# Optimization experiments

Measured on AMD Instinct MI355X. Metric: run time of the kernel, lower is better.

The kernel has to match this reference:

```python
import jax, jax.numpy as jnp
import numpy as np

N_NODES = 50000
N_EDGES = 500000
HIDDEN = 64
NUM_BASIS = 32
NUM_SH = 4  # (lmax+1)^2 with lmax=1


def _mlp(x, w1, b1, w2, b2):
    # Linear -> SiLU -> Linear, matching nn.Sequential(Linear, SiLU, Linear)
    return jax.nn.silu(x @ w1 + b1) @ w2 + b2


def setup_inputs() -> dict:
    key = jax.random.key(0)
    ks = jax.random.split(key, 10)
    scale_in = 1.0 / np.sqrt(NUM_BASIS)
    scale_h = 1.0 / np.sqrt(HIDDEN)
    return {
        "scalar": jax.random.normal(ks[0], (N_NODES, HIDDEN), dtype=jnp.float32),
        "vector": jax.random.normal(ks[1], (N_NODES, 3, HIDDEN), dtype=jnp.float32),
        "edge_sh": jax.random.normal(ks[2], (N_EDGES, NUM_SH), dtype=jnp.float32),
        "edge_length": jax.random.uniform(ks[3], (N_EDGES, NUM_BASIS), dtype=jnp.float32),
        "edge_index": jax.random.randint(ks[4], (2, N_EDGES), 0, N_NODES, dtype=jnp.int32),
        "sw1": jax.random.normal(ks[5], (NUM_BASIS, HIDDEN), dtype=jnp.float32) * scale_in,
        "sb1": jnp.zeros((HIDDEN,), dtype=jnp.float32),
        "sw2": jax.random.normal(ks[6], (HIDDEN, HIDDEN), dtype=jnp.float32) * scale_h,
        "sb2": jnp.zeros((HIDDEN,), dtype=jnp.float32),
        "vw1": jax.random.normal(ks[7], (NUM_BASIS, HIDDEN), dtype=jnp.float32) * scale_in,
        "vb1": jnp.zeros((HIDDEN,), dtype=jnp.float32),
        "vw2": jax.random.normal(ks[8], (HIDDEN, HIDDEN), dtype=jnp.float32) * scale_h,
        "vb2": jnp.zeros((HIDDEN,), dtype=jnp.float32),
    }


def reference(scalar, vector, edge_sh, edge_length, edge_index,
              sw1, sb1, sw2, sb2, vw1, vb1, vw2, vb2):
    # edge_sh is accepted (as in the torch forward signature) but unused.
    row, col = edge_index[0], edge_index[1]
    n = scalar.shape[0]

    # Edge-wise MLP weights from radial basis expansion: [E, hidden]
    scalar_weights = _mlp(edge_length, sw1, sb1, sw2, sb2)
    # Gather source-node scalars, weight, scatter-add to destination nodes.
    scalar_msg = scalar[col] * scalar_weights                   # [E, hidden]
    out_scalar = jax.ops.segment_sum(scalar_msg, row, num_segments=n)

    vector_weights = _mlp(edge_length, vw1, vb1, vw2, vb2)      # [E, hidden]
    vector_msg = vector[col] * vector_weights[:, None, :]       # [E, 3, hidden]
    out_vector = jax.ops.segment_sum(vector_msg, row, num_segments=n)

    return out_scalar, out_vector
```

## Files before the change

kernel.cpp:

```cpp
#include <hip/hip_runtime.h>

#define HIDDEN 64
#define NB 32
#define SCAN_BLOCK 1024
#define HSTR 72

typedef __attribute__((ext_vector_type(8))) short bf16x8;
typedef __attribute__((ext_vector_type(4))) float f32x4;

static __device__ __forceinline__ unsigned short f2bf(float x) {
    union { float f; unsigned u; } v; v.f = x;
    unsigned r = v.u + 0x7fffu + ((v.u >> 16) & 1u);
    return (unsigned short)(r >> 16);
}
static __device__ __forceinline__ float bf2f(unsigned short s) {
    union { unsigned u; float f; } v; v.u = ((unsigned)s) << 16;
    return v.f;
}

__global__ __launch_bounds__(256) void featpack_kernel(
    const float* __restrict__ scalar,
    const float* __restrict__ vector,
    ushort4* __restrict__ feat,
    int total)
{
    int i = blockIdx.x * 256 + threadIdx.x;
    if (i >= total) return;
    const int n = i >> 6, l = i & 63;
    const float* vp = vector + (size_t)n * 192 + l;
    ushort4 o;
    o.x = f2bf(scalar[i]);
    o.y = f2bf(vp[0]);
    o.z = f2bf(vp[64]);
    o.w = f2bf(vp[128]);
    feat[i] = o;
}

__global__ __launch_bounds__(SCAN_BLOCK) void scan_pass1(
    const int* __restrict__ counts, int* __restrict__ partial,
    int* __restrict__ blocksums, int N)
{
    __shared__ int tmp[SCAN_BLOCK];
    const int t = threadIdx.x;
    const int gid = blockIdx.x * SCAN_BLOCK + t;
    int v = (gid < N) ? counts[gid] : 0;
    tmp[t] = v;
    __syncthreads();
    for (int off = 1; off < SCAN_BLOCK; off <<= 1) {
        int x = (t >= off) ? tmp[t - off] : 0;
        __syncthreads();
        tmp[t] += x;
        __syncthreads();
    }
    if (gid < N) partial[gid] = tmp[t] - v;
    if (t == SCAN_BLOCK - 1) blocksums[blockIdx.x] = tmp[t];
}

__global__ __launch_bounds__(64) void scan_pass2(int* __restrict__ blocksums, int nb)
{
    const int t = threadIdx.x;
    int v = (t < nb) ? blocksums[t] : 0;
    int s = v;
    #pragma unroll
    for (int off = 1; off < 64; off <<= 1) {
        int x = __shfl_up(s, off, 64);
        if (t >= off) s += x;
    }
    if (t < nb) blocksums[t] = s - v;
}

__global__ __launch_bounds__(SCAN_BLOCK) void scan_pass3(
    const int* __restrict__ partial, const int* __restrict__ blocksums,
    int* __restrict__ offsets, int* __restrict__ cursors, int N, int E)
{
    const int gid = blockIdx.x * SCAN_BLOCK + threadIdx.x;
    if (gid < N) {
        int o = partial[gid] + blocksums[blockIdx.x];
        offsets[gid] = o;
        cursors[gid] = o;
    }
    if (blockIdx.x == 0 && threadIdx.x == 0) offsets[N] = E;
}

__global__ __launch_bounds__(256) void scatter_kernel(
    const int* __restrict__ edge_index, int* __restrict__ cursors,
    int2* __restrict__ pc, int E)
{
    int i = blockIdx.x * 256 + threadIdx.x;
    if (i < E) {
        int pos = atomicAdd(&cursors[edge_index[i]], 1);
        pc[pos] = make_int2(i, edge_index[E + i]);
    }
}

__global__ __launch_bounds__(256) void mlp_mfma_kernel(
    const float* __restrict__ edge_length,
    const int*   __restrict__ edge_index,
    int* __restrict__ counts,
    const float* __restrict__ sw1, const float* __restrict__ sb1,
    const float* __restrict__ sw2, const float* __restrict__ sb2,
    const float* __restrict__ vw1, const float* __restrict__ vb1,
    const float* __restrict__ vw2, const float* __restrict__ vb2,
    unsigned short* __restrict__ W,
    int E, int nchunks)
{
    __shared__ short Hs[4][64 * HSTR];

    const int t    = threadIdx.x;
    const int lane = t & 63;
    const int wid  = t >> 6;
    const int quad = lane >> 4;
    const int l16  = lane & 15;
    short* Hw = Hs[wid];

    const float* w1p[2] = {sw1, vw1};
    const float* b1p[2] = {sb1, vb1};
    const float* w2p[2] = {sw2, vw2};
    const float* b2p[2] = {sb2, vb2};

    bf16x8 w1f[2][4];
    bf16x8 w2f[2][2][4];
    float  b1v[2][4], b2v[2][4];
    #pragma unroll
    for (int m = 0; m < 2; ++m) {
        #pragma unroll
        for (int nt = 0; nt < 4; ++nt) {
            const int col = nt * 16 + l16;
            #pragma unroll
            for (int j = 0; j < 8; ++j)
                w1f[m][nt][j] = (short)f2bf(w1p[m][(quad * 8 + j) * HIDDEN + col]);
            #pragma unroll
            for (int kk = 0; kk < 2; ++kk) {
                #pragma unroll
                for (int j = 0; j < 8; ++j)
                    w2f[m][kk][nt][j] = (short)f2bf(w2p[m][(kk * 32 + quad * 8 + j) * HIDDEN + col]);
            }
            b1v[m][nt] = b1p[m][col];
            b2v[m][nt] = b2p[m][col];
        }
    }

    const int wave_g = blockIdx.x * 4 + wid;
    const int nwaves = gridDim.x * 4;

    for (int c = wave_g; c < nchunks; c += nwaves) {
        const int j0 = c * 64;

        {
            const int e = j0 + lane;
            if (e < E) atomicAdd(&counts[edge_index[e]], 1);
        }

        bf16x8 af[4];
        #pragma unroll
        for (int mt = 0; mt < 4; ++mt) {
            int e = j0 + mt * 16 + l16;
            if (e >= E) e = E - 1;
            const float* r = edge_length + (size_t)e * NB + quad * 8;
            float4 u0 = *(const float4*)r;
            float4 u1 = *(const float4*)(r + 4);
            af[mt][0] = (short)f2bf(u0.x); af[mt][1] = (short)f2bf(u0.y);
            af[mt][2] = (short)f2bf(u0.z); af[mt][3] = (short)f2bf(u0.w);
            af[mt][4] = (short)f2bf(u1.x); af[mt][5] = (short)f2bf(u1.y);
            af[mt][6] = (short)f2bf(u1.z); af[mt][7] = (short)f2bf(u1.w);
        }

        #pragma unroll
        for (int m = 0; m < 2; ++m) {
            #pragma unroll
            for (int mt = 0; mt < 4; ++mt) {
                #pragma unroll
                for (int nt = 0; nt < 4; ++nt) {
                    f32x4 cf = {b1v[m][nt], b1v[m][nt], b1v[m][nt], b1v[m][nt]};
                    cf = __builtin_amdgcn_mfma_f32_16x16x32_bf16(af[mt], w1f[m][nt], cf, 0, 0, 0);
                    #pragma unroll
                    for (int r4 = 0; r4 < 4; ++r4) {
                        float x = cf[r4];
                        x = x / (1.0f + __expf(-x));
                        const int row = mt * 16 + quad * 4 + r4;
                        Hw[row * HSTR + nt * 16 + l16] = (short)f2bf(x);
                    }
                }
            }

            #pragma unroll
            for (int mt = 0; mt < 4; ++mt) {
                const int arow = mt * 16 + l16;
                bf16x8 a0 = *(const bf16x8*)(Hw + arow * HSTR + quad * 8);
                bf16x8 a1 = *(const bf16x8*)(Hw + arow * HSTR + 32 + quad * 8);
                #pragma unroll
                for (int nt = 0; nt < 4; ++nt) {
                    f32x4 cf = {b2v[m][nt], b2v[m][nt], b2v[m][nt], b2v[m][nt]};
                    cf = __builtin_amdgcn_mfma_f32_16x16x32_bf16(a1, w2f[m][1][nt], cf, 0, 0, 0);
                    cf = __builtin_amdgcn_mfma_f32_16x16x32_bf16(a0, w2f[m][0][nt], cf, 0, 0, 0);
                    #pragma unroll
                    for (int r4 = 0; r4 < 4; ++r4) {
                        const int row = mt * 16 + quad * 4 + r4;
                        Hw[row * HSTR + nt * 16 + l16] = (short)f2bf(cf[r4]);
                    }
                }
            }

            #pragma unroll
            for (int i = 0; i < 8; ++i) {
                const int row = i * 8 + (lane >> 3);
                bf16x8 v = *(const bf16x8*)(Hw + row * HSTR + (lane & 7) * 8);
                if (j0 + row < E)
                    *(bf16x8*)(W + (size_t)(j0 + row) * 128 + m * 64 + (lane & 7) * 8) = v;
            }
        }
    }
}

__global__ __launch_bounds__(256) void node_kernel_feat(
    const ushort4* __restrict__ feat,
    const int* __restrict__ offsets,
    const int2* __restrict__ pc,
    const unsigned short* __restrict__ W,
    float* __restrict__ out_scalar,
    float* __restrict__ out_vector,
    int N)
{
    const int lane = threadIdx.x & 63;
    const int wave = blockIdx.x * 4 + (threadIdx.x >> 6);
    const int nw   = gridDim.x * 4;

    for (int n = wave; n < N; n += nw) {
        const int beg = offsets[n];
        const int end = offsets[n + 1];

        float as = 0.0f, a0 = 0.0f, a1 = 0.0f, a2 = 0.0f;
        float ws = 0, wv = 0, s = 0, v0 = 0, v1 = 0, v2 = 0;

        if (beg < end) {
            const int2 p = pc[beg];
            const unsigned short* wp = W + (size_t)p.x * 128;
            ws = bf2f(wp[lane]); wv = bf2f(wp[64 + lane]);
            const ushort4 f = feat[(size_t)p.y * 64 + lane];
            s = bf2f(f.x); v0 = bf2f(f.y); v1 = bf2f(f.z); v2 = bf2f(f.w);
        }

        for (int j = beg; j < end; ++j) {
            const int jn = (j + 1 < end) ? j + 1 : j;
            const int2 p = pc[jn];
            const unsigned short* wp = W + (size_t)p.x * 128;
            const float wsn = bf2f(wp[lane]);
            const float wvn = bf2f(wp[64 + lane]);
            const ushort4 f = feat[(size_t)p.y * 64 + lane];
            const float sn  = bf2f(f.x);
            const float v0n = bf2f(f.y);
            const float v1n = bf2f(f.z);
            const float v2n = bf2f(f.w);

            as = fmaf(s,  ws, as);
            a0 = fmaf(v0, wv, a0);
            a1 = fmaf(v1, wv, a1);
            a2 = fmaf(v2, wv, a2);

            ws = wsn; wv = wvn; s = sn; v0 = v0n; v1 = v1n; v2 = v2n;
        }

        out_scalar[(size_t)n * HIDDEN + lane] = as;
        float* ov = out_vector + (size_t)n * 3 * HIDDEN;
        ov[lane]       = a0;
        ov[64 + lane]  = a1;
        ov[128 + lane] = a2;
    }
}

__global__ __launch_bounds__(256) void node_kernel_f32(
    const float* __restrict__ scalar,
    const float* __restrict__ vector,
    const int* __restrict__ offsets,
    const int2* __restrict__ pc,
    const unsigned short* __restrict__ W,
    float* __restrict__ out_scalar,
    float* __restrict__ out_vector,
    int N)
{
    const int lane = threadIdx.x & 63;
    const int wave = blockIdx.x * 4 + (threadIdx.x >> 6);
    const int nw   = gridDim.x * 4;

    for (int n = wave; n < N; n += nw) {
        const int beg = offsets[n];
        const int end = offsets[n + 1];
        float as = 0.0f, a0 = 0.0f, a1 = 0.0f, a2 = 0.0f;
        for (int j = beg; j < end; ++j) {
            const int2 p = pc[j];
            const unsigned short* wp = W + (size_t)p.x * 128;
            const float w_s = bf2f(wp[lane]);
            const float w_v = bf2f(wp[64 + lane]);
            const float* sp = scalar + (size_t)p.y * HIDDEN;
            const float* vp = vector + (size_t)p.y * 3 * HIDDEN;
            as = fmaf(sp[lane],       w_s, as);
            a0 = fmaf(vp[lane],       w_v, a0);
            a1 = fmaf(vp[64 + lane],  w_v, a1);
            a2 = fmaf(vp[128 + lane], w_v, a2);
        }
        out_scalar[(size_t)n * HIDDEN + lane] = as;
        float* ov = out_vector + (size_t)n * 3 * HIDDEN;
        ov[lane]       = a0;
        ov[64 + lane]  = a1;
        ov[128 + lane] = a2;
    }
}

extern "C" void kernel_launch(void* const* d_in, const int* in_sizes, int n_in,
                              void* d_out, int out_size, void* d_ws, size_t ws_size,
                              hipStream_t stream) {
    const float* scalar      = (const float*)d_in[0];
    const float* vector      = (const float*)d_in[1];
    const float* edge_length = (const float*)d_in[3];
    const int*   edge_index  = (const int*)d_in[4];
    const float* sw1 = (const float*)d_in[5];
    const float* sb1 = (const float*)d_in[6];
    const float* sw2 = (const float*)d_in[7];
    const float* sb2 = (const float*)d_in[8];
    const float* vw1 = (const float*)d_in[9];
    const float* vb1 = (const float*)d_in[10];
    const float* vw2 = (const float*)d_in[11];
    const float* vb2 = (const float*)d_in[12];

    const int N = in_sizes[0] / HIDDEN;
    const int E = in_sizes[4] / 2;

    float* out_scalar = (float*)d_out;
    float* out_vector = (float*)d_out + (size_t)N * HIDDEN;

    size_t off = 0;
    unsigned short* W = (unsigned short*)d_ws;
    off += (size_t)E * 128 * 2;
    int2* pc = (int2*)((char*)d_ws + off);
    off += (size_t)E * 8;
    int* ib = (int*)((char*)d_ws + off);
    int* counts    = ib;
    int* partial   = ib + N;
    int* offsets   = ib + 2 * N;
    int* cursors   = ib + 3 * N + 1;
    int* blocksums = ib + 4 * N + 1;
    off += ((size_t)4 * N + 1 + 64) * 4;
    off = (off + 15) & ~(size_t)15;
    ushort4* feat = (ushort4*)((char*)d_ws + off);
    const bool use_feat = (off + (size_t)N * 64 * 8) <= ws_size;

    hipMemsetAsync(counts, 0, (size_t)N * sizeof(int), stream);

    const int egrid = (E + 255) / 256;

    if (use_feat) {
        const int total = N * 64;
        featpack_kernel<<<(total + 255) / 256, 256, 0, stream>>>(
            scalar, vector, feat, total);
    }

    const int nchunks = (E + 63) / 64;
    mlp_mfma_kernel<<<512, 256, 0, stream>>>(
        edge_length, edge_index, counts,
        sw1, sb1, sw2, sb2, vw1, vb1, vw2, vb2,
        W, E, nchunks);

    const int nb = (N + SCAN_BLOCK - 1) / SCAN_BLOCK;
    scan_pass1<<<nb, SCAN_BLOCK, 0, stream>>>(counts, partial, blocksums, N);
    scan_pass2<<<1, 64, 0, stream>>>(blocksums, nb);
    scan_pass3<<<nb, SCAN_BLOCK, 0, stream>>>(partial, blocksums, offsets, cursors, N, E);
    scatter_kernel<<<egrid, 256, 0, stream>>>(edge_index, cursors, pc, E);

    const int ngrid = (N + 3) / 4;
    if (use_feat) {
        node_kernel_feat<<<ngrid, 256, 0, stream>>>(
            feat, offsets, pc, W, out_scalar, out_vector, N);
    } else {
        node_kernel_f32<<<ngrid, 256, 0, stream>>>(
            scalar, vector, offsets, pc, W, out_scalar, out_vector, N);
    }
}
```

Before: 335.4 us.

## Restructure edge MLP kernel: split MLPs across waves, keep hidden layer in registers

Each block's four waves now split as two chunk slots times two MLPs (scalar or vector), so each wave holds the weights of only one MLP. The GEMMs are transposed (weights as the A operand, edges as B), which lets the first-layer SiLU output be packed straight into bf16 registers as the second GEMM's operand instead of going through LDS. SiLU now uses a hardware reciprocal, bf16 conversion uses packed intrinsics, and the grid covers all chunks (one pass per slot) instead of a fixed 512 blocks. The edge_length loads are duplicated across the two MLP waves, and the approximate reciprocal slightly changes numerics.

```diff
diff --git a/kernel.cpp b/kernel.cpp
--- a/kernel.cpp
+++ b/kernel.cpp
@@ -1,4 +1,5 @@
 #include <hip/hip_runtime.h>
+#include <hip/hip_bf16.h>
 
 #define HIDDEN 64
 #define NB 32
@@ -17,12 +18,18 @@
     union { unsigned u; float f; } v; v.u = ((unsigned)s) << 16;
     return v.f;
 }
+static __device__ __forceinline__ unsigned pk2(float a, float b) {
+    __hip_bfloat162 h = __float22bfloat162_rn(make_float2(a, b));
+    unsigned u; __builtin_memcpy(&u, &h, 4); return u;
+}
+static __device__ __forceinline__ float fast_silu(float x) {
+    float e = __expf(-x);
+    return x * __builtin_amdgcn_rcpf(1.0f + e);
+}
 
 __global__ __launch_bounds__(256) void featpack_kernel(
-    const float* __restrict__ scalar,
-    const float* __restrict__ vector,
-    ushort4* __restrict__ feat,
-    int total)
+    const float* __restrict__ scalar, const float* __restrict__ vector,
+    ushort4* __restrict__ feat, int total)
 {
     int i = blockIdx.x * 256 + threadIdx.x;
     if (i >= total) return;
@@ -109,105 +116,97 @@
     const int t    = threadIdx.x;
     const int lane = t & 63;
     const int wid  = t >> 6;
+    const int slot = wid & 1;
+    const int m    = wid >> 1;
     const int quad = lane >> 4;
     const int l16  = lane & 15;
     short* Hw = Hs[wid];
 
-    const float* w1p[2] = {sw1, vw1};
-    const float* b1p[2] = {sb1, vb1};
-    const float* w2p[2] = {sw2, vw2};
-    const float* b2p[2] = {sb2, vb2};
-
-    bf16x8 w1f[2][4];
-    bf16x8 w2f[2][2][4];
-    float  b1v[2][4], b2v[2][4];
+    const float* w1 = m ? vw1 : sw1;
+    const float* b1 = m ? vb1 : sb1;
+    const float* w2 = m ? vw2 : sw2;
+    const float* b2 = m ? vb2 : sb2;
+
+    bf16x8 w1a[4];
+    bf16x8 a2f[2][4];
+    float4 b1f[4], b2f[4];
     #pragma unroll
-    for (int m = 0; m < 2; ++m) {
-        #pragma unroll
-        for (int nt = 0; nt < 4; ++nt) {
-            const int col = nt * 16 + l16;
+    for (int mt = 0; mt < 4; ++mt) {
+        const int col = mt * 16 + l16;
+        #pragma unroll
+        for (int j = 0; j < 8; ++j)
+            w1a[mt][j] = (short)f2bf(w1[(quad * 8 + j) * HIDDEN + col]);
+        #pragma unroll
+        for (int kk = 0; kk < 2; ++kk)
             #pragma unroll
-            for (int j = 0; j < 8; ++j)
-                w1f[m][nt][j] = (short)f2bf(w1p[m][(quad * 8 + j) * HIDDEN + col]);
-            #pragma unroll
-            for (int kk = 0; kk < 2; ++kk) {
-                #pragma unroll
-                for (int j = 0; j < 8; ++j)
-                    w2f[m][kk][nt][j] = (short)f2bf(w2p[m][(kk * 32 + quad * 8 + j) * HIDDEN + col]);
+            for (int j = 0; j < 8; ++j) {
+                const int h = 16 * (2 * kk + (j >> 2)) + 4 * quad + (j & 3);
+                a2f[kk][mt][j] = (short)f2bf(w2[h * HIDDEN + col]);
             }
-            b1v[m][nt] = b1p[m][col];
-            b2v[m][nt] = b2p[m][col];
-        }
-    }
-
-    const int wave_g = blockIdx.x * 4 + wid;
-    const int nwaves = gridDim.x * 4;
-
-    for (int c = wave_g; c < nchunks; c += nwaves) {
+        b1f[mt] = *(const float4*)(b1 + mt * 16 + quad * 4);
+        b2f[mt] = *(const float4*)(b2 + mt * 16 + quad * 4);
+    }
+
+    const int stride = gridDim.x * 2;
+
+    for (int c = blockIdx.x * 2 + slot; c < nchunks; c += stride) {
         const int j0 = c * 64;
 
-        {
+        if (m == 0) {
             const int e = j0 + lane;
             if (e < E) atomicAdd(&counts[edge_index[e]], 1);
         }
 
         bf16x8 af[4];
         #pragma unroll
-        for (int mt = 0; mt < 4; ++mt) {
-            int e = j0 + mt * 16 + l16;
+        for (int nt = 0; nt < 4; ++nt) {
+            int e = j0 + nt * 16 + l16;
             if (e >= E) e = E - 1;
             const float* r = edge_length + (size_t)e * NB + quad * 8;
             float4 u0 = *(const float4*)r;
             float4 u1 = *(const float4*)(r + 4);
-            af[mt][0] = (short)f2bf(u0.x); af[mt][1] = (short)f2bf(u0.y);
-            af[mt][2] = (short)f2bf(u0.z); af[mt][3] = (short)f2bf(u0.w);
-            af[mt][4] = (short)f2bf(u1.x); af[mt][5] = (short)f2bf(u1.y);
-            af[mt][6] = (short)f2bf(u1.z); af[mt][7] = (short)f2bf(u1.w);
-        }
-
-        #pragma unroll
-        for (int m = 0; m < 2; ++m) {
+            union { bf16x8 v; unsigned u[4]; } p;
+            p.u[0] = pk2(u0.x, u0.y); p.u[1] = pk2(u0.z, u0.w);
+            p.u[2] = pk2(u1.x, u1.y); p.u[3] = pk2(u1.z, u1.w);
+            af[nt] = p.v;
+        }
+
+        #pragma unroll
+        for (int nt = 0; nt < 4; ++nt) {
+            float h[4][4];
             #pragma unroll
             for (int mt = 0; mt < 4; ++mt) {
+                f32x4 cf = {b1f[mt].x, b1f[mt].y, b1f[mt].z, b1f[mt].w};
+                cf = __builtin_amdgcn_mfma_f32_16x16x32_bf16(w1a[mt], af[nt], cf, 0, 0, 0);
                 #pragma unroll
-                for (int nt = 0; nt < 4; ++nt) {
-                    f32x4 cf = {b1v[m][nt], b1v[m][nt], b1v[m][nt], b1v[m][nt]};
-                    cf = __builtin_amdgcn_mfma_f32_16x16x32_bf16(af[mt], w1f[m][nt], cf, 0, 0, 0);
-                    #pragma unroll
-                    for (int r4 = 0; r4 < 4; ++r4) {
-                        float x = cf[r4];
-                        x = x / (1.0f + __expf(-x));
-                        const int row = mt * 16 + quad * 4 + r4;
-                        Hw[row * HSTR + nt * 16 + l16] = (short)f2bf(x);
-                    }
-                }
+                for (int r4 = 0; r4 < 4; ++r4)
+                    h[mt][r4] = fast_silu(cf[r4]);
             }
+
+            union { bf16x8 v; unsigned u[4]; } bf0, bf1;
+            bf0.u[0] = pk2(h[0][0], h[0][1]); bf0.u[1] = pk2(h[0][2], h[0][3]);
+            bf0.u[2] = pk2(h[1][0], h[1][1]); bf0.u[3] = pk2(h[1][2], h[1][3]);
+            bf1.u[0] = pk2(h[2][0], h[2][1]); bf1.u[1] = pk2(h[2][2], h[2][3]);
+            bf1.u[2] = pk2(h[3][0], h[3][1]); bf1.u[3] = pk2(h[3][2], h[3][3]);
 
             #pragma unroll
             for (int mt = 0; mt < 4; ++mt) {
-                const int arow = mt * 16 + l16;
-                bf16x8 a0 = *(const bf16x8*)(Hw + arow * HSTR + quad * 8);
-                bf16x8 a1 = *(const bf16x8*)(Hw + arow * HSTR + 32 + quad * 8);
-                #pragma unroll
-                for (int nt = 0; nt < 4; ++nt) {
-                    f32x4 cf = {b2v[m][nt], b2v[m][nt], b2v[m][nt], b2v[m][nt]};
-                    cf = __builtin_amdgcn_mfma_f32_16x16x32_bf16(a1, w2f[m][1][nt], cf, 0, 0, 0);
-                    cf = __builtin_amdgcn_mfma_f32_16x16x32_bf16(a0, w2f[m][0][nt], cf, 0, 0, 0);
-                    #pragma unroll
-                    for (int r4 = 0; r4 < 4; ++r4) {
-                        const int row = mt * 16 + quad * 4 + r4;
-                        Hw[row * HSTR + nt * 16 + l16] = (short)f2bf(cf[r4]);
-                    }
-                }
+                f32x4 cf = {b2f[mt].x, b2f[mt].y, b2f[mt].z, b2f[mt].w};
+                cf = __builtin_amdgcn_mfma_f32_16x16x32_bf16(a2f[0][mt], bf0.v, cf, 0, 0, 0);
+                cf = __builtin_amdgcn_mfma_f32_16x16x32_bf16(a2f[1][mt], bf1.v, cf, 0, 0, 0);
+                const unsigned u0 = pk2(cf[0], cf[1]);
+                const unsigned u1 = pk2(cf[2], cf[3]);
+                *(uint2*)(Hw + (nt * 16 + l16) * HSTR + mt * 16 + quad * 4) =
+                    make_uint2(u0, u1);
             }
-
-            #pragma unroll
-            for (int i = 0; i < 8; ++i) {
-                const int row = i * 8 + (lane >> 3);
-                bf16x8 v = *(const bf16x8*)(Hw + row * HSTR + (lane & 7) * 8);
-                if (j0 + row < E)
-                    *(bf16x8*)(W + (size_t)(j0 + row) * 128 + m * 64 + (lane & 7) * 8) = v;
-            }
+        }
+
+        #pragma unroll
+        for (int i = 0; i < 8; ++i) {
+            const int row = i * 8 + (lane >> 3);
+            bf16x8 v = *(const bf16x8*)(Hw + row * HSTR + (lane & 7) * 8);
+            if (j0 + row < E)
+                *(bf16x8*)(W + (size_t)(j0 + row) * 128 + m * 64 + (lane & 7) * 8) = v;
         }
     }
 }
@@ -355,7 +354,8 @@
     }
 
     const int nchunks = (E + 63) / 64;
-    mlp_mfma_kernel<<<512, 256, 0, stream>>>(
+    const int agrid   = (nchunks + 1) / 2;
+    mlp_mfma_kernel<<<agrid, 256, 0, stream>>>(
         edge_length, edge_index, counts,
         sw1, sb1, sw2, sb2, vw1, vb1, vw2, vb2,
         W, E, nchunks);
```

Result: no change. 337.2 us (+0.5%).
